# Performance work log

Hardware: AMD Instinct MI355X
Metric: run time of the kernel (lower is better)

Reference implementation:

```python
import jax, jax.numpy as jnp
import numpy as np
from jax import lax

HID = 32  # hardcoded hid_dim in the module

def setup_inputs() -> dict:
    key = jax.random.key(0)
    ks = jax.random.split(key, 12)
    B, HIST, C, F = 512, 24, 184, 17
    PRED = 24
    IN_DIM = HIST + F  # 41
    inp = {
        "pm25_hist": jax.random.normal(ks[0], (B, HIST, C, 1), jnp.float32),
        "feature": jax.random.normal(ks[1], (B, HIST + PRED, C, F), jnp.float32),
        "time_feature": jax.random.normal(ks[2], (B, HIST + PRED, 4), jnp.float32),
        # fc_in: Linear(in_dim, 32)
        "W_in": jax.random.normal(ks[3], (HID, IN_DIM), jnp.float32) / np.sqrt(IN_DIM),
        "b_in": jnp.zeros((HID,), jnp.float32),
        # LSTMCell(32, 32): gate order i, f, g, o
        "W_ih": jax.random.normal(ks[4], (4 * HID, HID), jnp.float32) / np.sqrt(HID),
        "W_hh": jax.random.normal(ks[5], (4 * HID, HID), jnp.float32) / np.sqrt(HID),
        "b_ih": jnp.zeros((4 * HID,), jnp.float32),
        "b_hh": jnp.zeros((4 * HID,), jnp.float32),
        # fc_out: Linear(32, 1)
        "W_out": jax.random.normal(ks[6], (1, HID), jnp.float32) / np.sqrt(HID),
        "b_out": jnp.zeros((1,), jnp.float32),
    }
    return inp

def _forward(pm25_hist, feature, W_in, b_in, W_ih, W_hh, b_ih, b_hh, W_out, b_out):
    B, HIST, C, _ = pm25_hist.shape
    PRED = feature.shape[1] - HIST
    # torch: pm25_hist.reshape(B, C, -1) -- raw row-major reinterpret, same in jnp
    xn0 = pm25_hist.reshape(B, C, HIST)
    h0 = jnp.zeros((B * C, HID), pm25_hist.dtype)
    c0 = jnp.zeros((B * C, HID), pm25_hist.dtype)
    # future features, time-major for scan: [PRED, B, C, F]
    feats = jnp.moveaxis(feature[:, HIST:HIST + PRED], 1, 0)

    def step(carry, feat_t):
        xn, h, c = carry
        x = jnp.concatenate([xn, feat_t], axis=-1)          # [B, C, in_dim]
        x = x @ W_in.T + b_in                               # [B, C, HID]
        xf = x.reshape(B * C, HID)
        gates = xf @ W_ih.T + b_ih + h @ W_hh.T + b_hh      # [B*C, 4*HID]
        i, f, g, o = jnp.split(gates, 4, axis=-1)
        i = jax.nn.sigmoid(i); f = jax.nn.sigmoid(f)
        g = jnp.tanh(g);       o = jax.nn.sigmoid(o)
        c = f * c + i * g
        h = o * jnp.tanh(c)
        pred = h.reshape(B, C, HID) @ W_out.T + b_out       # [B, C, 1]
        xn = jnp.concatenate([xn[:, :, 1:], pred], axis=-1)
        return (xn, h, c), pred

    _, preds = lax.scan(step, (xn0, h0, c0), feats)
    return jnp.moveaxis(preds, 0, 1)  # [B, PRED, C, 1]

def reference(pm25_hist, feature, time_feature, W_in, b_in, W_ih, W_hh, b_ih, b_hh, W_out, b_out):
    # time_feature is accepted but unused, matching the torch module
    return _forward(pm25_hist, feature, W_in, b_in, W_ih, W_hh, b_ih, b_hh, W_out, b_out)
```

## Files before the change

### kernel.cpp

```cpp
#include <hip/hip_runtime.h>
#include <hip/hip_bf16.h>


#define BN     512
#define HISTN  24
#define CNN    184
#define FN     17
#define PREDN  24
#define HIDN   32
#define INN    41
#define CELLS  (BN * CNN)
#define FROW   (CNN * FN)
#define PMROW  (HISTN * CNN)

typedef __attribute__((ext_vector_type(8))) short  short8;
typedef __attribute__((ext_vector_type(4))) float  float4v;

#define MFMA_B16(a, b, c) __builtin_amdgcn_mfma_f32_16x16x32_bf16(a, b, c, 0, 0, 0)

__device__ __forceinline__ short f2bf(float f) {
  union { float f; unsigned u; } v; v.f = f;
  unsigned r = v.u + 0x7fffu + ((v.u >> 16) & 1u);
  return (short)(r >> 16);
}

__device__ __forceinline__ float fast_sigmoid(float x) {
  float e = __expf(-x);
  return __builtin_amdgcn_rcpf(1.0f + e);
}
__device__ __forceinline__ float fast_tanh(float x) {
  float e = __expf(2.0f * x);
  return 1.0f - 2.0f * __builtin_amdgcn_rcpf(1.0f + e);
}

__device__ __forceinline__ int swz(int m, int k) {
  return (((k >> 3) ^ (m & 7)) << 3) | (k & 7);
}
__device__ __forceinline__ short8 rdfrag(const short* rowp, int m, int octl) {
  return *(const short8*)(rowp + ((octl ^ (m & 7)) << 3));
}

__global__ __launch_bounds__(256, 2)
void lstm_fused(const float* __restrict__ pm25,
                const float* __restrict__ feat,
                const float* __restrict__ W_in,  const float* __restrict__ b_in,
                const float* __restrict__ W_ih,  const float* __restrict__ W_hh,
                const float* __restrict__ b_ih,  const float* __restrict__ b_hh,
                const float* __restrict__ W_out, const float* __restrict__ b_out,
                float* __restrict__ out)
{
  __shared__ __align__(16) short Xs[64][64];
  __shared__ __align__(16) short Zs[64][64];
  __shared__ short buf[64][48];

  const int tid   = threadIdx.x;
  const int w     = tid >> 6;
  const int lane  = tid & 63;
  const int q     = lane >> 4;
  const int c0    = lane & 15;
  const int mb    = w << 4;
  const int cell0 = blockIdx.x << 6;

  short8 WzB[2][8];
  #pragma unroll
  for (int ks = 0; ks < 2; ks++) {
    #pragma unroll
    for (int nt = 0; nt < 8; nt++) {
      short8 f;
      const int g = nt * 16 + c0;
      #pragma unroll
      for (int j = 0; j < 8; j++) {
        const int k = ks * 32 + q * 8 + j;
        const float v = (k < 32) ? W_ih[g * 32 + k] : W_hh[g * 32 + (k - 32)];
        f[j] = f2bf(v);
      }
      WzB[ks][nt] = f;
    }
  }
  short8 WxB[2][2];
  #pragma unroll
  for (int ks = 0; ks < 2; ks++) {
    #pragma unroll
    for (int nt = 0; nt < 2; nt++) {
      short8 f;
      const int j2 = nt * 16 + c0;
      #pragma unroll
      for (int j = 0; j < 8; j++) {
        const int k = ks * 32 + q * 8 + j;
        f[j] = (k < INN) ? f2bf(W_in[j2 * INN + k]) : (short)0;
      }
      WxB[ks][nt] = f;
    }
  }
  float bias_i[2], bias_f[2], bias_g[2], bias_o[2], binr[2], woutr[2];
  #pragma unroll
  for (int s = 0; s < 2; s++) {
    const int j = s * 16 + c0;
    bias_i[s] = b_ih[j]      + b_hh[j];
    bias_f[s] = b_ih[32 + j] + b_hh[32 + j];
    bias_g[s] = b_ih[64 + j] + b_hh[64 + j];
    bias_o[s] = b_ih[96 + j] + b_hh[96 + j];
    binr[s]   = b_in[j];
    woutr[s]  = W_out[j];
  }
  const float bo = b_out[0];

  const int cl  = mb + (lane >> 2);
  const int sub = lane & 3;
  const int cg  = cell0 + cl;
  const int bb  = cg / CNN, cc = cg % CNN;
  const float* featBase = feat + ((size_t)(bb * 48 + HISTN)) * FROW + cc * FN;

  {
    const float* src = pm25 + bb * PMROW + cc * HISTN;
    #pragma unroll
    for (int kk = 0; kk < 6; kk++) {
      const int k = sub * 6 + kk;
      buf[cl][k] = f2bf(src[k]);
    }
    for (int k = 41 + sub; k < 64; k += 4) Xs[cl][swz(cl, k)] = 0;
    for (int k = 32 + sub; k < 64; k += 4) Zs[cl][swz(cl, k)] = 0;
  }

  int outB[4], outC[4];
  #pragma unroll
  for (int r = 0; r < 4; r++) {
    const int cgr = cell0 + mb + q * 4 + r;
    outB[r] = cgr / CNN;
    outC[r] = cgr % CNN;
  }

  float cst[2][4];
  #pragma unroll
  for (int s = 0; s < 2; s++)
    #pragma unroll
    for (int r = 0; r < 4; r++) cst[s][r] = 0.f;

  float fv[5];
  #pragma unroll
  for (int i = 0; i < 5; i++) {
    const int f = sub * 5 + i;
    fv[i] = (f < FN) ? featBase[f] : 0.f;
  }

  #pragma unroll 1
  for (int t = 0; t < PREDN; t++) {
    #pragma unroll
    for (int kk = 0; kk < 6; kk++) {
      const int k = sub * 6 + kk;
      Xs[cl][swz(cl, k)] = buf[cl][t + k];
    }
    #pragma unroll
    for (int i = 0; i < 5; i++) {
      const int f = sub * 5 + i;
      if (f < FN) Xs[cl][swz(cl, 24 + f)] = f2bf(fv[i]);
    }
    if (t < PREDN - 1) {
      const float* p = featBase + (size_t)(t + 1) * FROW;
      #pragma unroll
      for (int i = 0; i < 5; i++) {
        const int f = sub * 5 + i;
        fv[i] = (f < FN) ? p[f] : 0.f;
      }
    }

    const short* xrow = &Xs[mb + c0][0];
    const short8 xa = rdfrag(xrow, mb + c0, q);
    const short8 xb = rdfrag(xrow, mb + c0, 4 + q);
    float4v xh[2];
    #pragma unroll
    for (int nt = 0; nt < 2; nt++) {
      float4v a = {0.f, 0.f, 0.f, 0.f};
      a = MFMA_B16(xa, WxB[0][nt], a);
      a = MFMA_B16(xb, WxB[1][nt], a);
      xh[nt] = a;
    }
    #pragma unroll
    for (int s = 0; s < 2; s++) {
      const int j = s * 16 + c0;
      #pragma unroll
      for (int r = 0; r < 4; r++) {
        const int m = mb + q * 4 + r;
        Zs[m][swz(m, j)] = f2bf(xh[s][r] + binr[s]);
      }
    }

    const short* zrow = &Zs[mb + c0][0];
    const short8 za = rdfrag(zrow, mb + c0, q);
    const short8 zb = rdfrag(zrow, mb + c0, 4 + q);
    float4v acc[8];
    #pragma unroll
    for (int nt = 0; nt < 8; nt++) {
      float4v a = {0.f, 0.f, 0.f, 0.f};
      a = MFMA_B16(za, WzB[0][nt], a);
      a = MFMA_B16(zb, WzB[1][nt], a);
      acc[nt] = a;
    }

    float part[4] = {0.f, 0.f, 0.f, 0.f};
    #pragma unroll
    for (int s = 0; s < 2; s++) {
      const int j = s * 16 + c0;
      #pragma unroll
      for (int r = 0; r < 4; r++) {
        const float iv  = fast_sigmoid(acc[0 + s][r] + bias_i[s]);
        const float ff  = fast_sigmoid(acc[2 + s][r] + bias_f[s]);
        const float gv  = fast_tanh   (acc[4 + s][r] + bias_g[s]);
        const float ov  = fast_sigmoid(acc[6 + s][r] + bias_o[s]);
        const float cn  = ff * cst[s][r] + iv * gv;
        cst[s][r] = cn;
        const float hv = ov * fast_tanh(cn);
        const int m = mb + q * 4 + r;
        Zs[m][swz(m, 32 + j)] = f2bf(hv);
        part[r] += woutr[s] * hv;
      }
    }
    #pragma unroll
    for (int r = 0; r < 4; r++) {
      float p = part[r];
      p += __shfl_xor(p, 1);
      p += __shfl_xor(p, 2);
      p += __shfl_xor(p, 4);
      p += __shfl_xor(p, 8);
      part[r] = p;
    }
    if (c0 == 0) {
      #pragma unroll
      for (int r = 0; r < 4; r++) {
        const float pr = part[r] + bo;
        out[(outB[r] * PREDN + t) * CNN + outC[r]] = pr;
        buf[mb + q * 4 + r][24 + t] = f2bf(pr);
      }
    }
  }
}

extern "C" void kernel_launch(void* const* d_in, const int* in_sizes, int n_in,
                              void* d_out, int out_size, void* d_ws, size_t ws_size,
                              hipStream_t stream) {
  (void)in_sizes; (void)n_in; (void)out_size; (void)d_ws; (void)ws_size;
  const float* pm25  = (const float*)d_in[0];
  const float* feat  = (const float*)d_in[1];
  const float* W_in  = (const float*)d_in[3];
  const float* b_in  = (const float*)d_in[4];
  const float* W_ih  = (const float*)d_in[5];
  const float* W_hh  = (const float*)d_in[6];
  const float* b_ih  = (const float*)d_in[7];
  const float* b_hh  = (const float*)d_in[8];
  const float* W_out = (const float*)d_in[9];
  const float* b_out = (const float*)d_in[10];
  float* out = (float*)d_out;

  lstm_fused<<<dim3(CELLS / 64), dim3(256), 0, stream>>>(
      pm25, feat, W_in, b_in, W_ih, W_hh, b_ih, b_hh, W_out, b_out, out);
}
```

Baseline: 519.5 us.

## Fold input projection into LSTM gate weights and use MFMA for output projection

A small setup kernel precomputes W_ih·W_in and the combined biases into workspace, so the per-step input projection MFMA and its LDS round-trip are removed and gates come straight from [x, h] via three MFMAs (K=32+32+16). The output projection is done with an MFMA instead of a shuffle reduction. The history window is kept in packed registers and shifted each step, and occupancy is raised to 4 blocks per SIMD group. Numerics change slightly because the fused weight is rounded to bf16, and there is an extra kernel launch.

```diff
diff --git a/kernel.cpp b/kernel.cpp
--- a/kernel.cpp
+++ b/kernel.cpp
@@ -7,23 +7,29 @@
 #define CNN    184
 #define FN     17
 #define PREDN  24
-#define HIDN   32
-#define INN    41
 #define CELLS  (BN * CNN)
 #define FROW   (CNN * FN)
 #define PMROW  (HISTN * CNN)
-
-typedef __attribute__((ext_vector_type(8))) short  short8;
-typedef __attribute__((ext_vector_type(4))) float  float4v;
-
-#define MFMA_B16(a, b, c) __builtin_amdgcn_mfma_f32_16x16x32_bf16(a, b, c, 0, 0, 0)
+#define ZSTR   88
+#define WCW    48
+
+typedef __attribute__((ext_vector_type(8))) short  s8v;
+typedef __attribute__((ext_vector_type(4))) short  s4v;
+typedef __attribute__((ext_vector_type(4))) float  f4v;
+
+#define MFMA32(a, b, c) __builtin_amdgcn_mfma_f32_16x16x32_bf16(a, b, c, 0, 0, 0)
+#define MFMA16(a, b, c) __builtin_amdgcn_mfma_f32_16x16x16bf16_1k(a, b, c, 0, 0, 0)
 
 __device__ __forceinline__ short f2bf(float f) {
   union { float f; unsigned u; } v; v.f = f;
   unsigned r = v.u + 0x7fffu + ((v.u >> 16) & 1u);
   return (short)(r >> 16);
 }
-
+__device__ __forceinline__ unsigned pack_bf2(float a, float b) {
+  union { __hip_bfloat162 h; unsigned u; } v;
+  v.h = __float22bfloat162_rn(make_float2(a, b));
+  return v.u;
+}
 __device__ __forceinline__ float fast_sigmoid(float x) {
   float e = __expf(-x);
   return __builtin_amdgcn_rcpf(1.0f + e);
@@ -33,24 +39,36 @@
   return 1.0f - 2.0f * __builtin_amdgcn_rcpf(1.0f + e);
 }
 
-__device__ __forceinline__ int swz(int m, int k) {
-  return (((k >> 3) ^ (m & 7)) << 3) | (k & 7);
-}
-__device__ __forceinline__ short8 rdfrag(const short* rowp, int m, int octl) {
-  return *(const short8*)(rowp + ((octl ^ (m & 7)) << 3));
-}
-
-__global__ __launch_bounds__(256, 2)
+__global__ void setup_wc(const float* __restrict__ W_in, const float* __restrict__ b_in,
+                         const float* __restrict__ W_ih, const float* __restrict__ b_ih,
+                         const float* __restrict__ b_hh, float* __restrict__ ws) {
+  const int idx = blockIdx.x * 256 + threadIdx.x;
+  if (idx < 128 * WCW) {
+    const int g = idx / WCW, k = idx % WCW;
+    float s = 0.f;
+    if (k < 41) {
+      #pragma unroll
+      for (int j = 0; j < 32; j++) s += W_ih[g * 32 + j] * W_in[j * 41 + k];
+    }
+    ws[idx] = s;
+  } else if (idx < 128 * WCW + 128) {
+    const int g = idx - 128 * WCW;
+    float s = b_ih[g] + b_hh[g];
+    #pragma unroll
+    for (int j = 0; j < 32; j++) s += W_ih[g * 32 + j] * b_in[j];
+    ws[128 * WCW + g] = s;
+  }
+}
+
+__global__ __launch_bounds__(256, 4)
 void lstm_fused(const float* __restrict__ pm25,
                 const float* __restrict__ feat,
-                const float* __restrict__ W_in,  const float* __restrict__ b_in,
-                const float* __restrict__ W_ih,  const float* __restrict__ W_hh,
-                const float* __restrict__ b_ih,  const float* __restrict__ b_hh,
+                const float* __restrict__ W_hh,
                 const float* __restrict__ W_out, const float* __restrict__ b_out,
+                const float* __restrict__ ws,
                 float* __restrict__ out)
 {
-  __shared__ __align__(16) short Xs[64][64];
-  __shared__ __align__(16) short Zs[64][64];
+  __shared__ __align__(16) short Zs[64][ZSTR];
   __shared__ short buf[64][48];
 
   const int tid   = threadIdx.x;
@@ -61,71 +79,69 @@
   const int mb    = w << 4;
   const int cell0 = blockIdx.x << 6;
 
-  short8 WzB[2][8];
-  #pragma unroll
-  for (int ks = 0; ks < 2; ks++) {
-    #pragma unroll
-    for (int nt = 0; nt < 8; nt++) {
-      short8 f;
-      const int g = nt * 16 + c0;
-      #pragma unroll
-      for (int j = 0; j < 8; j++) {
-        const int k = ks * 32 + q * 8 + j;
-        const float v = (k < 32) ? W_ih[g * 32 + k] : W_hh[g * 32 + (k - 32)];
-        f[j] = f2bf(v);
-      }
-      WzB[ks][nt] = f;
-    }
-  }
-  short8 WxB[2][2];
-  #pragma unroll
-  for (int ks = 0; ks < 2; ks++) {
-    #pragma unroll
-    for (int nt = 0; nt < 2; nt++) {
-      short8 f;
-      const int j2 = nt * 16 + c0;
-      #pragma unroll
-      for (int j = 0; j < 8; j++) {
-        const int k = ks * 32 + q * 8 + j;
-        f[j] = (k < INN) ? f2bf(W_in[j2 * INN + k]) : (short)0;
-      }
-      WxB[ks][nt] = f;
-    }
-  }
-  float bias_i[2], bias_f[2], bias_g[2], bias_o[2], binr[2], woutr[2];
+  const float* wc = ws;
+  const float* wb = ws + 128 * WCW;
+
+  s8v WzA[8], WzB[8]; s4v WzC[8];
+  #pragma unroll
+  for (int nt = 0; nt < 8; nt++) {
+    const int g = ((nt >> 1) << 5) + (c0 << 1) + (nt & 1);
+    s8v f0, f1;
+    #pragma unroll
+    for (int j = 0; j < 8; j++) {
+      const int k0 = q * 8 + j;
+      f0[j] = f2bf(wc[g * WCW + k0]);
+      const int k1 = 32 + q * 8 + j;
+      const float v = (k1 < 48) ? wc[g * WCW + k1] : W_hh[g * 32 + (k1 - 48)];
+      f1[j] = f2bf(v);
+    }
+    WzA[nt] = f0; WzB[nt] = f1;
+    s4v f2;
+    #pragma unroll
+    for (int j = 0; j < 4; j++) f2[j] = f2bf(W_hh[g * 32 + 16 + q * 4 + j]);
+    WzC[nt] = f2;
+  }
+  s8v WoB;
+  #pragma unroll
+  for (int j = 0; j < 8; j++) WoB[j] = (c0 == 0) ? f2bf(W_out[q * 8 + j]) : (short)0;
+
+  float bi[2], bfg[2], bgg[2], bog[2];
   #pragma unroll
   for (int s = 0; s < 2; s++) {
-    const int j = s * 16 + c0;
-    bias_i[s] = b_ih[j]      + b_hh[j];
-    bias_f[s] = b_ih[32 + j] + b_hh[32 + j];
-    bias_g[s] = b_ih[64 + j] + b_hh[64 + j];
-    bias_o[s] = b_ih[96 + j] + b_hh[96 + j];
-    binr[s]   = b_in[j];
-    woutr[s]  = W_out[j];
-  }
-  const float bo = b_out[0];
-
-  const int cl  = mb + (lane >> 2);
-  const int sub = lane & 3;
-  const int cg  = cell0 + cl;
-  const int bb  = cg / CNN, cc = cg % CNN;
+    const int g = (c0 << 1) + s;
+    bi[s]  = wb[g];
+    bfg[s] = wb[32 + g];
+    bgg[s] = wb[64 + g];
+    bog[s] = wb[96 + g];
+  }
+  const float bout = b_out[0];
+  f4v pinit;
+  #pragma unroll
+  for (int r = 0; r < 4; r++) pinit[r] = (c0 == 0) ? bout : 0.f;
+
+  const int cl   = mb + (lane >> 2);
+  const int sub  = lane & 3;
+  const int sub6 = sub * 6, sub4 = sub * 4;
+  const int cg   = cell0 + cl;
+  const int bb   = cg / CNN, cc = cg % CNN;
   const float* featBase = feat + ((size_t)(bb * 48 + HISTN)) * FROW + cc * FN;
-
-  {
-    const float* src = pm25 + bb * PMROW + cc * HISTN;
-    #pragma unroll
-    for (int kk = 0; kk < 6; kk++) {
-      const int k = sub * 6 + kk;
-      buf[cl][k] = f2bf(src[k]);
-    }
-    for (int k = 41 + sub; k < 64; k += 4) Xs[cl][swz(cl, k)] = 0;
-    for (int k = 32 + sub; k < 64; k += 4) Zs[cl][swz(cl, k)] = 0;
-  }
+  const float* src = pm25 + bb * PMROW + cc * HISTN;
+
+  unsigned w0 = pack_bf2(src[sub6 + 0], src[sub6 + 1]);
+  unsigned w1 = pack_bf2(src[sub6 + 2], src[sub6 + 3]);
+  unsigned w2 = pack_bf2(src[sub6 + 4], src[sub6 + 5]);
+  *(unsigned*)&buf[cl][sub6 + 0] = w0;
+  *(unsigned*)&buf[cl][sub6 + 2] = w1;
+  *(unsigned*)&buf[cl][sub6 + 4] = w2;
+
+  Zs[cl][41 + sub] = 0;
+  if (sub < 3) Zs[cl][45 + sub] = 0;
+  { s8v zz = 0; *(s8v*)&Zs[cl][48 + sub * 8] = zz; }
 
   int outB[4], outC[4];
   #pragma unroll
   for (int r = 0; r < 4; r++) {
-    const int cgr = cell0 + mb + q * 4 + r;
+    const int cgr = cell0 + mb + (q << 2) + r;
     outB[r] = cgr / CNN;
     outC[r] = cgr % CNN;
   }
@@ -138,107 +154,80 @@
 
   float fv[5];
   #pragma unroll
-  for (int i = 0; i < 5; i++) {
-    const int f = sub * 5 + i;
-    fv[i] = (f < FN) ? featBase[f] : 0.f;
-  }
+  for (int i = 0; i < 5; i++)
+    if (i < 4 || sub == 3) fv[i] = featBase[sub4 + i];
 
   #pragma unroll 1
   for (int t = 0; t < PREDN; t++) {
-    #pragma unroll
-    for (int kk = 0; kk < 6; kk++) {
-      const int k = sub * 6 + kk;
-      Xs[cl][swz(cl, k)] = buf[cl][t + k];
-    }
-    #pragma unroll
-    for (int i = 0; i < 5; i++) {
-      const int f = sub * 5 + i;
-      if (f < FN) Xs[cl][swz(cl, 24 + f)] = f2bf(fv[i]);
-    }
+    *(unsigned*)&Zs[cl][sub6 + 0] = w0;
+    *(unsigned*)&Zs[cl][sub6 + 2] = w1;
+    *(unsigned*)&Zs[cl][sub6 + 4] = w2;
+    *(unsigned*)&Zs[cl][24 + sub4 + 0] = pack_bf2(fv[0], fv[1]);
+    *(unsigned*)&Zs[cl][24 + sub4 + 2] = pack_bf2(fv[2], fv[3]);
+    if (sub == 3) Zs[cl][40] = f2bf(fv[4]);
     if (t < PREDN - 1) {
       const float* p = featBase + (size_t)(t + 1) * FROW;
       #pragma unroll
-      for (int i = 0; i < 5; i++) {
-        const int f = sub * 5 + i;
-        fv[i] = (f < FN) ? p[f] : 0.f;
-      }
-    }
-
-    const short* xrow = &Xs[mb + c0][0];
-    const short8 xa = rdfrag(xrow, mb + c0, q);
-    const short8 xb = rdfrag(xrow, mb + c0, 4 + q);
-    float4v xh[2];
-    #pragma unroll
-    for (int nt = 0; nt < 2; nt++) {
-      float4v a = {0.f, 0.f, 0.f, 0.f};
-      a = MFMA_B16(xa, WxB[0][nt], a);
-      a = MFMA_B16(xb, WxB[1][nt], a);
-      xh[nt] = a;
-    }
+      for (int i = 0; i < 5; i++)
+        if (i < 4 || sub == 3) fv[i] = p[sub4 + i];
+    }
+
+    const short* zrow = &Zs[mb + c0][0];
+    const s8v za = *(const s8v*)&zrow[q * 8];
+    const s8v zb = *(const s8v*)&zrow[32 + q * 8];
+    const s4v zc = *(const s4v*)&zrow[64 + q * 4];
+    f4v acc[8];
+    #pragma unroll
+    for (int nt = 0; nt < 8; nt++) {
+      f4v a = {0.f, 0.f, 0.f, 0.f};
+      a = MFMA32(za, WzA[nt], a);
+      a = MFMA32(zb, WzB[nt], a);
+      a = MFMA16(zc, WzC[nt], a);
+      acc[nt] = a;
+    }
+
+    float hv0[4], hv1[4];
     #pragma unroll
     for (int s = 0; s < 2; s++) {
-      const int j = s * 16 + c0;
       #pragma unroll
       for (int r = 0; r < 4; r++) {
-        const int m = mb + q * 4 + r;
-        Zs[m][swz(m, j)] = f2bf(xh[s][r] + binr[s]);
-      }
-    }
-
-    const short* zrow = &Zs[mb + c0][0];
-    const short8 za = rdfrag(zrow, mb + c0, q);
-    const short8 zb = rdfrag(zrow, mb + c0, 4 + q);
-    float4v acc[8];
-    #pragma unroll
-    for (int nt = 0; nt < 8; nt++) {
-      float4v a = {0.f, 0.f, 0.f, 0.f};
-      a = MFMA_B16(za, WzB[0][nt], a);
-      a = MFMA_B16(zb, WzB[1][nt], a);
-      acc[nt] = a;
-    }
-
-    float part[4] = {0.f, 0.f, 0.f, 0.f};
-    #pragma unroll
-    for (int s = 0; s < 2; s++) {
-      const int j = s * 16 + c0;
-      #pragma unroll
-      for (int r = 0; r < 4; r++) {
-        const float iv  = fast_sigmoid(acc[0 + s][r] + bias_i[s]);
-        const float ff  = fast_sigmoid(acc[2 + s][r] + bias_f[s]);
-        const float gv  = fast_tanh   (acc[4 + s][r] + bias_g[s]);
-        const float ov  = fast_sigmoid(acc[6 + s][r] + bias_o[s]);
-        const float cn  = ff * cst[s][r] + iv * gv;
+        const float iv = fast_sigmoid(acc[0 + s][r] + bi[s]);
+        const float ff = fast_sigmoid(acc[2 + s][r] + bfg[s]);
+        const float gv = fast_tanh   (acc[4 + s][r] + bgg[s]);
+        const float ov = fast_sigmoid(acc[6 + s][r] + bog[s]);
+        const float cn = ff * cst[s][r] + iv * gv;
         cst[s][r] = cn;
         const float hv = ov * fast_tanh(cn);
-        const int m = mb + q * 4 + r;
-        Zs[m][swz(m, 32 + j)] = f2bf(hv);
-        part[r] += woutr[s] * hv;
+        if (s == 0) hv0[r] = hv; else hv1[r] = hv;
       }
     }
     #pragma unroll
     for (int r = 0; r < 4; r++) {
-      float p = part[r];
-      p += __shfl_xor(p, 1);
-      p += __shfl_xor(p, 2);
-      p += __shfl_xor(p, 4);
-      p += __shfl_xor(p, 8);
-      part[r] = p;
-    }
+      const int m = mb + (q << 2) + r;
+      *(unsigned*)&Zs[m][48 + (c0 << 1)] = pack_bf2(hv0[r], hv1[r]);
+    }
+
+    const s8v zh = *(const s8v*)&zrow[48 + q * 8];
+    const f4v pacc = MFMA32(zh, WoB, pinit);
     if (c0 == 0) {
       #pragma unroll
       for (int r = 0; r < 4; r++) {
-        const float pr = part[r] + bo;
-        out[(outB[r] * PREDN + t) * CNN + outC[r]] = pr;
-        buf[mb + q * 4 + r][24 + t] = f2bf(pr);
+        out[(outB[r] * PREDN + t) * CNN + outC[r]] = pacc[r];
+        buf[mb + (q << 2) + r][24 + t] = f2bf(pacc[r]);
       }
     }
+
+    const short nb = buf[cl][t + 6 + sub6];
+    w0 = (w0 >> 16) | (w1 << 16);
+    w1 = (w1 >> 16) | (w2 << 16);
+    w2 = (w2 >> 16) | ((unsigned)(unsigned short)nb << 16);
   }
 }
 
 extern "C" void kernel_launch(void* const* d_in, const int* in_sizes, int n_in,
                               void* d_out, int out_size, void* d_ws, size_t ws_size,
                               hipStream_t stream) {
-  (void)in_sizes; (void)n_in; (void)out_size; (void)d_ws; (void)ws_size;
+  (void)in_sizes; (void)n_in; (void)out_size; (void)ws_size;
   const float* pm25  = (const float*)d_in[0];
   const float* feat  = (const float*)d_in[1];
   const float* W_in  = (const float*)d_in[3];
@@ -249,8 +238,10 @@
   const float* b_hh  = (const float*)d_in[8];
   const float* W_out = (const float*)d_in[9];
   const float* b_out = (const float*)d_in[10];
+  float* ws  = (float*)d_ws;
   float* out = (float*)d_out;
 
+  setup_wc<<<dim3(25), dim3(256), 0, stream>>>(W_in, b_in, W_ih, b_ih, b_hh, ws);
   lstm_fused<<<dim3(CELLS / 64), dim3(256), 0, stream>>>(
-      pm25, feat, W_in, b_in, W_ih, W_hh, b_ih, b_hh, W_out, b_out, out);
-}
+      pm25, feat, W_hh, W_out, b_out, ws, out);
+}
```

Result: slower. 809.9 us (+55.9%).
